# Optimization experiments

Measured on AMD Instinct MI355X. Metric: run time of the kernel, lower is better.

The kernel has to match this reference:

```python
import jax, jax.numpy as jnp
import numpy as np

DIM = 1024
HEADS = 16
DIM_HEAD = 64
INNER = HEADS * DIM_HEAD  # 1024
SCALE = DIM_HEAD ** -0.5


def setup_inputs() -> dict:
    key = jax.random.key(0)
    k1, k2, k3, k4 = jax.random.split(key, 4)
    B, N = 4, 2048
    x = jax.random.normal(k1, (B, N, DIM), dtype=jnp.float32)
    # Linear weights stored as [in, out] so y = x @ W (+ b)
    W_qkv = jax.random.normal(k2, (DIM, 3 * INNER), dtype=jnp.float32) * (DIM ** -0.5)
    W_out = jax.random.normal(k3, (INNER, DIM), dtype=jnp.float32) * (INNER ** -0.5)
    b_out = jax.random.normal(k4, (DIM,), dtype=jnp.float32) * 0.01
    return {"x": x, "W_qkv": W_qkv, "W_out": W_out, "b_out": b_out}


def reference(x, W_qkv, W_out, b_out):
    B, N, _ = x.shape
    qkv = x @ W_qkv  # [B, N, 3*INNER]
    q, k, v = jnp.split(qkv, 3, axis=-1)
    # [B, N, H, Dh] -> [B, H, N, Dh]
    reshape = lambda t: t.reshape(B, N, HEADS, DIM_HEAD).transpose(0, 2, 1, 3)
    q, k, v = reshape(q), reshape(k), reshape(v)
    dots = jnp.einsum("bhqd,bhkd->bhqk", q, k) * SCALE  # [B,H,N,N]
    attn = jax.nn.softmax(dots, axis=-1)
    out = jnp.einsum("bhqk,bhkd->bhqd", attn, v)  # [B,H,N,Dh]
    out = out.transpose(0, 2, 1, 3).reshape(B, N, INNER)
    return out @ W_out + b_out
```

## Files before the change

kernel.cpp:

```cpp
#include <hip/hip_runtime.h>


typedef _Float16 half8 __attribute__((ext_vector_type(8)));
typedef __fp16 fp16v2 __attribute__((ext_vector_type(2)));
typedef float floatx4 __attribute__((ext_vector_type(4)));
typedef unsigned short u16;

struct __align__(8) U16x4 { u16 x, y, z, w; };

__device__ __forceinline__ u16 f2h(float f) {
  union { _Float16 h; u16 u; } cv;
  cv.h = (_Float16)f;
  return cv.u;
}

__device__ __forceinline__ void g2l16(const void* g, void* l) {
  __builtin_amdgcn_global_load_lds(
      (const __attribute__((address_space(1))) void*)g,
      (__attribute__((address_space(3))) void*)l, 16, 0, 0);
}

__device__ __forceinline__ int swz(int c) { return (c & 3) ^ ((c >> 3) & 3); }

__global__ __launch_bounds__(256) void prep(const float* __restrict__ x,
                                            u16* __restrict__ Xh,
                                            const float* __restrict__ Wqkv,
                                            u16* __restrict__ Wqkvt,
                                            const float* __restrict__ Wout,
                                            u16* __restrict__ Woutt) {
  __shared__ u16 ls[64][72];
  const int bid = blockIdx.x;
  const int tid = threadIdx.x;
  if (bid < 4096) {
    long long base = ((long long)bid * 256 + tid) * 8;
    float4 a = *(const float4*)(x + base);
    float4 b = *(const float4*)(x + base + 4);
    U16x4 u0 = {f2h(a.x), f2h(a.y), f2h(a.z), f2h(a.w)};
    U16x4 u1 = {f2h(b.x), f2h(b.y), f2h(b.z), f2h(b.w)};
    *(U16x4*)(Xh + base) = u0;
    *(U16x4*)(Xh + base + 4) = u1;
    return;
  }
  const float* in;
  u16* out;
  int N, tile;
  if (bid < 4096 + 768) { in = Wqkv; out = Wqkvt; N = 3072; tile = bid - 4096; }
  else                  { in = Wout; out = Woutt; N = 1024; tile = bid - 4864; }
  const int K = 1024, nTK = 16;
  const int tk = tile % nTK, tn = tile / nTK;
#pragma unroll
  for (int i = 0; i < 4; ++i) {
    int idx = i * 256 + tid;
    int r = idx >> 4, c4 = (idx & 15) * 4;
    float4 v = *(const float4*)(in + (long long)(tk * 64 + r) * N + tn * 64 + c4);
    ls[r][c4 + 0] = f2h(v.x);
    ls[r][c4 + 1] = f2h(v.y);
    ls[r][c4 + 2] = f2h(v.z);
    ls[r][c4 + 3] = f2h(v.w);
  }
  __syncthreads();
#pragma unroll
  for (int i = 0; i < 4; ++i) {
    int idx = i * 256 + tid;
    int nr = idx >> 4, kc4 = (idx & 15) * 4;
    U16x4 u = {ls[kc4 + 0][nr], ls[kc4 + 1][nr], ls[kc4 + 2][nr], ls[kc4 + 3][nr]};
    *(U16x4*)(out + (long long)(tn * 64 + nr) * K + tk * 64 + kc4) = u;
  }
}

template <int EPI>
__global__ __launch_bounds__(256, 3) void gemm_f16(const u16* __restrict__ A,
                                                   const u16* __restrict__ Bt,
                                                   u16* __restrict__ O0,
                                                   u16* __restrict__ O1,
                                                   u16* __restrict__ O2,
                                                   float* __restrict__ Of,
                                                   const float* __restrict__ bias) {
  __shared__ __attribute__((aligned(16))) u16 lsA[3 * 4096];
  __shared__ __attribute__((aligned(16))) u16 lsB[3 * 4096];
  const int tid = threadIdx.x;
  const int lane = tid & 63, wave = tid >> 6;
  const int l15 = lane & 15, quad = lane >> 4;
  const int rdoff = (quad ^ ((l15 >> 1) & 3)) * 8;
  const int wm = (wave >> 1) * 64, wn = (wave & 1) * 64;
  const int bm = blockIdx.x & 63, bn = blockIdx.x >> 6;

  const u16* gA[2];
  const u16* gB[2];
  int dst[2];
#pragma unroll
  for (int j = 0; j < 2; ++j) {
    int sl = j * 256 + tid;
    int r = sl >> 2, cc = sl & 3;
    int csw = (cc ^ ((r >> 1) & 3)) * 8;
    gA[j] = A + (long long)(bm * 128 + r) * 1024 + csw;
    gB[j] = Bt + (long long)(bn * 128 + r) * 1024 + csw;
    dst[j] = sl * 8;
  }

  floatx4 acc[4][4] = {};

#pragma unroll
  for (int t = 0; t < 2; ++t) {
#pragma unroll
    for (int j = 0; j < 2; ++j) g2l16(gA[j] + t * 32, lsA + t * 4096 + dst[j]);
#pragma unroll
    for (int j = 0; j < 2; ++j) g2l16(gB[j] + t * 32, lsB + t * 4096 + dst[j]);
  }
  asm volatile("s_waitcnt vmcnt(4)");
  __builtin_amdgcn_s_barrier();

  int cur = 0;
  for (int t = 0; t < 32; ++t) {
    const u16* bA = lsA + cur * 4096;
    const u16* bB = lsB + cur * 4096;
    half8 af[4], bf[4];
#pragma unroll
    for (int i = 0; i < 4; ++i)
      af[i] = *(const half8*)(bA + (wm + i * 16 + l15) * 32 + rdoff);
#pragma unroll
    for (int i = 0; i < 4; ++i)
      bf[i] = *(const half8*)(bB + (wn + i * 16 + l15) * 32 + rdoff);
    if (t < 30) {
      const int nb = cur ? cur - 1 : 2;
      const int ko = (t + 2) * 32;
#pragma unroll
      for (int j = 0; j < 2; ++j) g2l16(gA[j] + ko, lsA + nb * 4096 + dst[j]);
#pragma unroll
      for (int j = 0; j < 2; ++j) g2l16(gB[j] + ko, lsB + nb * 4096 + dst[j]);
    }
    __builtin_amdgcn_s_barrier();
    asm volatile("s_waitcnt lgkmcnt(0)");
#pragma unroll
    for (int mt = 0; mt < 4; ++mt)
#pragma unroll
      for (int nt = 0; nt < 4; ++nt)
        acc[mt][nt] = __builtin_amdgcn_mfma_f32_16x16x32_f16(af[mt], bf[nt],
                                                             acc[mt][nt], 0, 0, 0);
    if (t < 30)       asm volatile("s_waitcnt vmcnt(4)");
    else if (t == 30) asm volatile("s_waitcnt vmcnt(0)");
    __builtin_amdgcn_s_barrier();
    cur = cur == 2 ? 0 : cur + 1;
  }

  if (EPI == 0) {
    const float slq = 0.125f * 1.44269504088896f;
#pragma unroll
    for (int mt = 0; mt < 4; ++mt) {
      int gm = bm * 128 + wm + mt * 16 + quad * 4;
      int b = gm >> 11, n0 = gm & 2047;
#pragma unroll
      for (int nt = 0; nt < 4; ++nt) {
        int gc = bn * 128 + wn + nt * 16 + l15;
        int tsel = gc >> 10, hd = gc & 1023, h = hd >> 6, d = hd & 63;
        long long bh = (long long)(b * 16 + h);
        if (tsel == 2) {
          U16x4 u = {f2h(acc[mt][nt][0]), f2h(acc[mt][nt][1]),
                     f2h(acc[mt][nt][2]), f2h(acc[mt][nt][3])};
          *(U16x4*)(O2 + (bh * 64 + d) * 2048 + n0) = u;
        } else {
          float s = (tsel == 0) ? slq : 1.0f;
          u16* dstp = (tsel == 0 ? O0 : O1) + (bh * 2048 + n0) * 64 + d;
#pragma unroll
          for (int r = 0; r < 4; ++r) dstp[r * 64] = f2h(acc[mt][nt][r] * s);
        }
      }
    }
  } else {
#pragma unroll
    for (int mt = 0; mt < 4; ++mt) {
      int gm = bm * 128 + wm + mt * 16 + quad * 4;
#pragma unroll
      for (int nt = 0; nt < 4; ++nt) {
        int gc = bn * 128 + wn + nt * 16 + l15;
        float bv = bias[gc];
#pragma unroll
        for (int r = 0; r < 4; ++r)
          Of[(long long)(gm + r) * 1024 + gc] = acc[mt][nt][r] + bv;
      }
    }
  }
}

__global__ __launch_bounds__(256, 2) void attn_flash(const u16* __restrict__ Qh,
                                                     const u16* __restrict__ Kh,
                                                     const u16* __restrict__ Vt,
                                                     u16* __restrict__ Oh) {
  __shared__ __attribute__((aligned(16))) u16 lsK[2 * 2 * 64 * 32];
  __shared__ __attribute__((aligned(16))) u16 lsV[2 * 2 * 64 * 32];
  __shared__ __attribute__((aligned(16))) u16 lsP[4 * 64 * 32];
  const int tid = threadIdx.x;
  const int lane = tid & 63, wave = tid >> 6;
  const int l15 = lane & 15, quad = lane >> 4;
  const int sw = (l15 >> 1) & 3;
  const int qsw8 = (quad ^ sw) * 8;
  const int bh = blockIdx.x & 63, qt = blockIdx.x >> 6;
  const u16* Qb = Qh + ((long long)bh * 2048 + qt * 256) * 64;
  const u16* Kb = Kh + (long long)bh * 2048 * 64;
  const u16* Vb = Vt + (long long)bh * 64 * 2048;
  u16* lsPw = lsP + wave * 2048;

  half8 qb[4][2];
#pragma unroll
  for (int pass = 0; pass < 2; ++pass) {
#pragma unroll
    for (int i = 0; i < 4; ++i) {
      int c = i * 256 + tid;
      g2l16(Qb + (pass * 128 + ((c >> 2) & 127)) * 64 + (c >> 9) * 32 + swz(c) * 8,
            lsK + (i * 256 + wave * 64) * 8);
    }
    __syncthreads();
    if ((wave >> 1) == pass) {
      const int lrow = (wave & 1) * 64;
#pragma unroll
      for (int qt2 = 0; qt2 < 4; ++qt2)
#pragma unroll
        for (int ks = 0; ks < 2; ++ks)
          qb[qt2][ks] = *(const half8*)(lsK + ks * 4096 +
                                        (lrow + qt2 * 16 + l15) * 32 + qsw8);
    }
    __syncthreads();
  }

#pragma unroll
  for (int i = 0; i < 2; ++i) {
    int c = i * 256 + tid;
    g2l16(Kb + ((c >> 2) & 63) * 64 + (c >> 8) * 32 + swz(c) * 8,
          lsK + (i * 256 + wave * 64) * 8);
    g2l16(Vb + ((c >> 2) & 63) * 2048 + (c >> 8) * 32 + swz(c) * 8,
          lsV + (i * 256 + wave * 64) * 8);
  }

  half8 onesf;
#pragma unroll
  for (int j = 0; j < 8; ++j) onesf[j] = (_Float16)1.0f;

  floatx4 oacc[4][4] = {};
  floatx4 osum[4] = {};

  for (int kt = 0; kt < 32; ++kt) {
    const int cur = kt & 1;
    const u16* bufK = lsK + cur * 4096;
    const u16* bufV = lsV + cur * 4096;
    __syncthreads();
    if (kt < 31) {
      u16* nK = lsK + (1 - cur) * 4096;
      u16* nV = lsV + (1 - cur) * 4096;
#pragma unroll
      for (int i = 0; i < 2; ++i) {
        int c = i * 256 + tid;
        g2l16(Kb + (kt + 1) * 4096 + ((c >> 2) & 63) * 64 + (c >> 8) * 32 + swz(c) * 8,
              nK + (i * 256 + wave * 64) * 8);
        g2l16(Vb + ((c >> 2) & 63) * 2048 + (kt + 1) * 64 + (c >> 8) * 32 + swz(c) * 8,
              nV + (i * 256 + wave * 64) * 8);
      }
    }
#pragma unroll
    for (int ks4 = 0; ks4 < 2; ++ks4) {
      floatx4 sacc[2][4] = {};
      __builtin_amdgcn_s_setprio(1);
#pragma unroll
      for (int ks = 0; ks < 2; ++ks) {
#pragma unroll
        for (int h = 0; h < 2; ++h) {
          half8 kf = *(const half8*)(bufK + ks * 2048 + ((ks4 * 2 + h) * 16 + l15) * 32 + qsw8);
#pragma unroll
          for (int qt2 = 0; qt2 < 4; ++qt2)
            sacc[h][qt2] = __builtin_amdgcn_mfma_f32_16x16x32_f16(kf, qb[qt2][ks], sacc[h][qt2], 0, 0, 0);
        }
      }
      __builtin_amdgcn_s_setprio(0);
#pragma unroll
      for (int h = 0; h < 2; ++h) {
#pragma unroll
        for (int qt2 = 0; qt2 < 4; ++qt2) {
          float p0 = __builtin_amdgcn_exp2f(sacc[h][qt2][0]);
          float p1 = __builtin_amdgcn_exp2f(sacc[h][qt2][1]);
          float p2 = __builtin_amdgcn_exp2f(sacc[h][qt2][2]);
          float p3 = __builtin_amdgcn_exp2f(sacc[h][qt2][3]);
          union { fp16v2 h2; unsigned u; } lo, hi;
          lo.h2 = __builtin_amdgcn_cvt_pkrtz(p0, p1);
          hi.h2 = __builtin_amdgcn_cvt_pkrtz(p2, p3);
          uint2 pk = {lo.u, hi.u};
          *(uint2*)(lsPw + (qt2 * 16 + l15) * 32 +
                    (((2 * h + (quad >> 1)) ^ sw) * 8) + (quad & 1) * 4) = pk;
        }
      }
      half8 pa[4];
#pragma unroll
      for (int qt2 = 0; qt2 < 4; ++qt2)
        pa[qt2] = *(const half8*)(lsPw + (qt2 * 16 + l15) * 32 + qsw8);
      __builtin_amdgcn_s_setprio(1);
#pragma unroll
      for (int dt = 0; dt < 4; ++dt) {
        half8 vb = *(const half8*)(bufV + ks4 * 2048 + (dt * 16 + l15) * 32 + qsw8);
#pragma unroll
        for (int qt2 = 0; qt2 < 4; ++qt2)
          oacc[qt2][dt] = __builtin_amdgcn_mfma_f32_16x16x32_f16(pa[qt2], vb, oacc[qt2][dt], 0, 0, 0);
      }
#pragma unroll
      for (int qt2 = 0; qt2 < 4; ++qt2)
        osum[qt2] = __builtin_amdgcn_mfma_f32_16x16x32_f16(pa[qt2], onesf, osum[qt2], 0, 0, 0);
      __builtin_amdgcn_s_setprio(0);
    }
  }

  const int b = bh >> 4, h = bh & 15;
#pragma unroll
  for (int qt2 = 0; qt2 < 4; ++qt2) {
#pragma unroll
    for (int r = 0; r < 4; ++r) {
      float inv = 1.0f / osum[qt2][r];
      int qrow = qt * 256 + wave * 64 + qt2 * 16 + quad * 4 + r;
      long long rowbase = ((long long)b * 2048 + qrow) * 1024 + h * 64;
#pragma unroll
      for (int dt = 0; dt < 4; ++dt)
        Oh[rowbase + dt * 16 + l15] = f2h(oacc[qt2][dt][r] * inv);
    }
  }
}

extern "C" void kernel_launch(void* const* d_in, const int* in_sizes, int n_in,
                              void* d_out, int out_size, void* d_ws, size_t ws_size,
                              hipStream_t stream) {
  const float* x = (const float*)d_in[0];
  const float* Wqkv = (const float*)d_in[1];
  const float* Wout = (const float*)d_in[2];
  const float* bout = (const float*)d_in[3];
  float* out = (float*)d_out;

  char* ws = (char*)d_ws;
  u16* Xh = (u16*)(ws);
  u16* Wqkvt = (u16*)(ws + (16ll << 20));
  u16* Woutt = (u16*)(ws + (22ll << 20));
  u16* Qh = (u16*)(ws + (24ll << 20));
  u16* Kh = (u16*)(ws + (40ll << 20));
  u16* Vt = (u16*)(ws + (56ll << 20));
  u16* Oh = (u16*)(ws + (72ll << 20));

  prep<<<5120, 256, 0, stream>>>(x, Xh, Wqkv, Wqkvt, Wout, Woutt);
  gemm_f16<0><<<1536, 256, 0, stream>>>(Xh, Wqkvt, Qh, Kh, Vt, nullptr, nullptr);
  attn_flash<<<512, 256, 0, stream>>>(Qh, Kh, Vt, Oh);
  gemm_f16<1><<<512, 256, 0, stream>>>(Oh, Woutt, nullptr, nullptr, nullptr, out, bout);
}
```

Before: 245.7 us.

## Use 256x128 tiles with block swizzle for the QKV projection GEMM

Splits the templated GEMM into a dedicated QKV kernel and an output-projection kernel. The QKV kernel grows the M tile from 128 to 256 rows, with each wave computing 128x64 in two MFMA halves, which halves the B-operand reloads and doubles arithmetic per LDS byte. It also remaps block IDs across 8 groups to change L2 locality. The cost is more accumulator registers and more LDS per block (occupancy drops from 3 to 2 blocks per CU), and the grid shrinks to 768 blocks, which may hurt wave balance across CUs.

Measured after the change: 268.3 us. +9.2%, slower.

```diff
diff --git a/kernel.cpp b/kernel.cpp
--- a/kernel.cpp
+++ b/kernel.cpp
@@ -68,12 +68,120 @@
   }
 }
 
-template <int EPI>
-__global__ __launch_bounds__(256, 3) void gemm_f16(const u16* __restrict__ A,
+__global__ __launch_bounds__(256, 2) void qkv_gemm(const u16* __restrict__ A,
                                                    const u16* __restrict__ Bt,
                                                    u16* __restrict__ O0,
                                                    u16* __restrict__ O1,
-                                                   u16* __restrict__ O2,
+                                                   u16* __restrict__ O2) {
+  __shared__ __attribute__((aligned(16))) u16 lsA[3 * 8192];
+  __shared__ __attribute__((aligned(16))) u16 lsB[3 * 4096];
+  const int tid = threadIdx.x;
+  const int lane = tid & 63, wave = tid >> 6;
+  const int l15 = lane & 15, quad = lane >> 4;
+  const int rdoff = (quad ^ ((l15 >> 1) & 3)) * 8;
+  const int wm = (wave >> 1) * 128, wn = (wave & 1) * 64;
+  const int b = (blockIdx.x & 7) * 96 + (blockIdx.x >> 3);
+  const int bm = b & 31, bn = b >> 5;
+
+  const u16* gA[4];
+  const u16* gB[2];
+  int dA[4], dB[2];
+#pragma unroll
+  for (int j = 0; j < 4; ++j) {
+    int sl = j * 256 + tid;
+    int r = sl >> 2, cc = sl & 3;
+    gA[j] = A + (long long)(bm * 256 + r) * 1024 + (cc ^ ((r >> 1) & 3)) * 8;
+    dA[j] = sl * 8;
+  }
+#pragma unroll
+  for (int j = 0; j < 2; ++j) {
+    int sl = j * 256 + tid;
+    int r = sl >> 2, cc = sl & 3;
+    gB[j] = Bt + (long long)(bn * 128 + r) * 1024 + (cc ^ ((r >> 1) & 3)) * 8;
+    dB[j] = sl * 8;
+  }
+
+  floatx4 acc[8][4] = {};
+
+#pragma unroll
+  for (int t = 0; t < 2; ++t) {
+#pragma unroll
+    for (int j = 0; j < 4; ++j) g2l16(gA[j] + t * 32, lsA + t * 8192 + dA[j]);
+#pragma unroll
+    for (int j = 0; j < 2; ++j) g2l16(gB[j] + t * 32, lsB + t * 4096 + dB[j]);
+  }
+  asm volatile("s_waitcnt vmcnt(6)");
+  __builtin_amdgcn_s_barrier();
+
+  int cur = 0;
+  for (int t = 0; t < 32; ++t) {
+    const u16* bA = lsA + cur * 8192;
+    const u16* bB = lsB + cur * 4096;
+    half8 af[4], bf[4];
+#pragma unroll
+    for (int i = 0; i < 4; ++i)
+      bf[i] = *(const half8*)(bB + (wn + i * 16 + l15) * 32 + rdoff);
+#pragma unroll
+    for (int i = 0; i < 4; ++i)
+      af[i] = *(const half8*)(bA + (wm + i * 16 + l15) * 32 + rdoff);
+    if (t < 30) {
+      const int nb = cur ? cur - 1 : 2;
+      const int ko = (t + 2) * 32;
+#pragma unroll
+      for (int j = 0; j < 4; ++j) g2l16(gA[j] + ko, lsA + nb * 8192 + dA[j]);
+#pragma unroll
+      for (int j = 0; j < 2; ++j) g2l16(gB[j] + ko, lsB + nb * 4096 + dB[j]);
+    }
+    __builtin_amdgcn_s_barrier();
+    asm volatile("s_waitcnt lgkmcnt(0)");
+#pragma unroll
+    for (int i = 0; i < 4; ++i)
+#pragma unroll
+      for (int nt = 0; nt < 4; ++nt)
+        acc[i][nt] = __builtin_amdgcn_mfma_f32_16x16x32_f16(af[i], bf[nt],
+                                                            acc[i][nt], 0, 0, 0);
+    half8 ag[4];
+#pragma unroll
+    for (int i = 0; i < 4; ++i)
+      ag[i] = *(const half8*)(bA + (wm + 64 + i * 16 + l15) * 32 + rdoff);
+#pragma unroll
+    for (int i = 0; i < 4; ++i)
+#pragma unroll
+      for (int nt = 0; nt < 4; ++nt)
+        acc[4 + i][nt] = __builtin_amdgcn_mfma_f32_16x16x32_f16(ag[i], bf[nt],
+                                                                acc[4 + i][nt], 0, 0, 0);
+    if (t < 30)       asm volatile("s_waitcnt vmcnt(6)");
+    else if (t == 30) asm volatile("s_waitcnt vmcnt(0)");
+    __builtin_amdgcn_s_barrier();
+    cur = cur == 2 ? 0 : cur + 1;
+  }
+
+  const float slq = 0.125f * 1.44269504088896f;
+#pragma unroll
+  for (int mt = 0; mt < 8; ++mt) {
+    int gm = bm * 256 + wm + (mt >> 2) * 64 + (mt & 3) * 16 + quad * 4;
+    int bb = gm >> 11, n0 = gm & 2047;
+#pragma unroll
+    for (int nt = 0; nt < 4; ++nt) {
+      int gc = bn * 128 + wn + nt * 16 + l15;
+      int tsel = gc >> 10, hd = gc & 1023, h = hd >> 6, d = hd & 63;
+      long long bh = (long long)(bb * 16 + h);
+      if (tsel == 2) {
+        U16x4 u = {f2h(acc[mt][nt][0]), f2h(acc[mt][nt][1]),
+                   f2h(acc[mt][nt][2]), f2h(acc[mt][nt][3])};
+        *(U16x4*)(O2 + (bh * 64 + d) * 2048 + n0) = u;
+      } else {
+        float s = (tsel == 0) ? slq : 1.0f;
+        u16* dstp = (tsel == 0 ? O0 : O1) + (bh * 2048 + n0) * 64 + d;
+#pragma unroll
+        for (int r = 0; r < 4; ++r) dstp[r * 64] = f2h(acc[mt][nt][r] * s);
+      }
+    }
+  }
+}
+
+__global__ __launch_bounds__(256, 3) void out_gemm(const u16* __restrict__ A,
+                                                   const u16* __restrict__ Bt,
                                                    float* __restrict__ Of,
                                                    const float* __restrict__ bias) {
   __shared__ __attribute__((aligned(16))) u16 lsA[3 * 4096];
@@ -143,41 +251,16 @@
     cur = cur == 2 ? 0 : cur + 1;
   }
 
-  if (EPI == 0) {
-    const float slq = 0.125f * 1.44269504088896f;
-#pragma unroll
-    for (int mt = 0; mt < 4; ++mt) {
-      int gm = bm * 128 + wm + mt * 16 + quad * 4;
-      int b = gm >> 11, n0 = gm & 2047;
-#pragma unroll
-      for (int nt = 0; nt < 4; ++nt) {
-        int gc = bn * 128 + wn + nt * 16 + l15;
-        int tsel = gc >> 10, hd = gc & 1023, h = hd >> 6, d = hd & 63;
-        long long bh = (long long)(b * 16 + h);
-        if (tsel == 2) {
-          U16x4 u = {f2h(acc[mt][nt][0]), f2h(acc[mt][nt][1]),
-                     f2h(acc[mt][nt][2]), f2h(acc[mt][nt][3])};
-          *(U16x4*)(O2 + (bh * 64 + d) * 2048 + n0) = u;
-        } else {
-          float s = (tsel == 0) ? slq : 1.0f;
-          u16* dstp = (tsel == 0 ? O0 : O1) + (bh * 2048 + n0) * 64 + d;
-#pragma unroll
-          for (int r = 0; r < 4; ++r) dstp[r * 64] = f2h(acc[mt][nt][r] * s);
-        }
-      }
-    }
-  } else {
-#pragma unroll
-    for (int mt = 0; mt < 4; ++mt) {
-      int gm = bm * 128 + wm + mt * 16 + quad * 4;
-#pragma unroll
-      for (int nt = 0; nt < 4; ++nt) {
-        int gc = bn * 128 + wn + nt * 16 + l15;
-        float bv = bias[gc];
-#pragma unroll
-        for (int r = 0; r < 4; ++r)
-          Of[(long long)(gm + r) * 1024 + gc] = acc[mt][nt][r] + bv;
-      }
+#pragma unroll
+  for (int mt = 0; mt < 4; ++mt) {
+    int gm = bm * 128 + wm + mt * 16 + quad * 4;
+#pragma unroll
+    for (int nt = 0; nt < 4; ++nt) {
+      int gc = bn * 128 + wn + nt * 16 + l15;
+      float bv = bias[gc];
+#pragma unroll
+      for (int r = 0; r < 4; ++r)
+        Of[(long long)(gm + r) * 1024 + gc] = acc[mt][nt][r] + bv;
     }
   }
 }
@@ -339,7 +422,7 @@
   u16* Oh = (u16*)(ws + (72ll << 20));
 
   prep<<<5120, 256, 0, stream>>>(x, Xh, Wqkv, Wqkvt, Wout, Woutt);
-  gemm_f16<0><<<1536, 256, 0, stream>>>(Xh, Wqkvt, Qh, Kh, Vt, nullptr, nullptr);
+  qkv_gemm<<<768, 256, 0, stream>>>(Xh, Wqkvt, Qh, Kh, Vt);
   attn_flash<<<512, 256, 0, stream>>>(Qh, Kh, Vt, Oh);
-  gemm_f16<1><<<512, 256, 0, stream>>>(Oh, Woutt, nullptr, nullptr, nullptr, out, bout);
-}
+  out_gemm<<<512, 256, 0, stream>>>(Oh, Woutt, out, bout);
+}
```
